# Performance work log

Hardware: AMD Instinct MI355X
Metric: run time of the kernel (lower is better)

Reference implementation:

```python
import jax, jax.numpy as jnp
import numpy as np

B, DIM = 16384, 1024
H1, H2, H3 = 500, 200, 200


def setup_inputs() -> dict:
    key = jax.random.key(0)
    ks = jax.random.split(key, 16)
    s = 0.01
    return {
        "x": jax.random.normal(ks[0], (B, DIM), dtype=jnp.float32),
        "show_index": jax.random.randint(ks[1], (B,), 0, 100),
        "st": jax.random.normal(ks[2], (1000, 16), dtype=jnp.float32),
        # deep MLP params (shared across the two task heads, as in the source)
        "W1": jax.random.normal(ks[3], (DIM, H1), dtype=jnp.float32) * s,
        "b1": jnp.zeros((H1,), dtype=jnp.float32),
        "W2": jax.random.normal(ks[4], (H1, H2), dtype=jnp.float32) * s,
        "b2": jnp.zeros((H2,), dtype=jnp.float32),
        "W3": jax.random.normal(ks[5], (H2, H3), dtype=jnp.float32) * s,
        "b3": jnp.zeros((H3,), dtype=jnp.float32),
        # final sigmoid head on concat([emb(DIM), d3(H3)])
        "Wl": jax.random.normal(ks[6], (DIM + H3, 1), dtype=jnp.float32) * s,
        "bl": jnp.zeros((1,), dtype=jnp.float32),
        # per-(task, cross-layer) cross weights/biases: tf.random_normal stddev=0.01
        "cw": jax.random.normal(ks[7], (2, 3, DIM), dtype=jnp.float32) * s,
        "cb": jax.random.normal(ks[8], (2, 3, DIM), dtype=jnp.float32) * s,
    }


def reference(x, show_index, st, W1, b1, W2, b2, W3, b3, Wl, bl, cw, cb):
    # Deep part (same shared Dense layers each task -> compute once).
    d = jax.nn.relu(x @ W1 + b1)
    d = jax.nn.relu(d @ W2 + b2)
    d3 = jax.nn.relu(d @ W3 + b3)  # (B, H3)

    # cross_net: sum_i w[j] * x[b,i] * emb[b,j]  ==  x.sum(1) * emb[b,j] * w[j]
    # (collapsed form of the (B,dim,dim) outer product + axis-1 reduction)
    xsum = jnp.sum(x, axis=1, keepdims=True)  # (B, 1)
    preds = []
    for i in range(2):
        emb = x
        for j in range(3):
            emb = xsum * emb * cw[i, j] + cb[i, j] + x
        mid = jnp.concatenate([emb, d3], axis=-1)  # (B, DIM+H3)
        preds.append(jax.nn.sigmoid(mid @ Wl + bl))  # (B, 1)
    return tuple(preds)
```

## Files before the change

kernel.cpp:

```cpp
#include <hip/hip_runtime.h>
#include <hip/hip_bf16.h>
#include <math.h>

#define B_ROWS 16384
#define DIM 1024

typedef __attribute__((ext_vector_type(8))) short s16x8;
typedef __attribute__((ext_vector_type(4))) float f32x4;

static __device__ __forceinline__ unsigned short f2bf(float f) {
    union { float f; unsigned u; } v; v.f = f;
    unsigned r = v.u + 0x7FFF + ((v.u >> 16) & 1);
    return (unsigned short)(r >> 16);
}

static __device__ __forceinline__ unsigned cvt_pk_bf16(float lo, float hi) {
    unsigned r;
    asm volatile("v_cvt_pk_bf16_f32 %0, %1, %2" : "=v"(r) : "v"(lo), "v"(hi));
    return r;
}

static __device__ __forceinline__ void gload16(const unsigned short* g, unsigned short* l) {
    __builtin_amdgcn_global_load_lds(
        (const __attribute__((address_space(1))) unsigned int*)g,
        (__attribute__((address_space(3))) unsigned int*)l, 16, 0, 0);
}

__global__ __launch_bounds__(256) void prep(
    const float* __restrict__ W1, const float* __restrict__ W2,
    const float* __restrict__ W3,
    const float* __restrict__ cw, const float* __restrict__ cb,
    const float* __restrict__ Wl,
    unsigned short* __restrict__ W1b, unsigned short* __restrict__ W2b,
    unsigned short* __restrict__ W3b,
    float* __restrict__ czz) {
    __shared__ unsigned short tile[64][72];
    __shared__ float red[4][6];
    const int tid = threadIdx.x;
    const int blk = blockIdx.x;

    if (blk < 176) {
        const int w = blk;
        const float* src; unsigned short* dst;
        int kt, nt, Ksrc, Nsrc, ldDst;
        bool skipHi = false;
        if (w < 128)      { kt = w & 15;         nt = w >> 4;         src = W1; dst = W1b; Ksrc = 1024; Nsrc = 500; ldDst = 1024; skipHi = true; }
        else if (w < 160) { kt = (w - 128) & 7;  nt = (w - 128) >> 3; src = W2; dst = W2b; Ksrc = 500;  Nsrc = 200; ldDst = 512;  }
        else              { kt = (w - 160) & 3;  nt = (w - 160) >> 2; src = W3; dst = W3b; Ksrc = 200;  Nsrc = 200; ldDst = 256;  }
        const int k0 = kt << 6, n0 = nt << 6;
        {
            const int r = tid >> 2, c0 = (tid & 3) << 4;
            const int kk = k0 + r;
#pragma unroll
            for (int i = 0; i < 16; ++i) {
                const int nn = n0 + c0 + i;
                const float v = (kk < Ksrc && nn < Nsrc) ? src[(size_t)kk * Nsrc + nn] : 0.f;
                tile[r][c0 + i] = f2bf(v);
            }
        }
        __syncthreads();
        {
            const int n = tid >> 2, kc = (tid & 3) << 4;
            if (!(skipHi && (n0 + n) >= 500)) {
                unsigned short* o = dst + (size_t)(n0 + n) * ldDst + k0 + kc;
#pragma unroll
                for (int i = 0; i < 16; ++i) o[i] = tile[kc + i][n];
            }
        }
    } else if (blk == 176) {
#pragma unroll
        for (int q = 0; q < 4; ++q) {
            const int k = tid * 4 + q;
            const float wl = Wl[k];
            const float a1 = cw[k],         a2 = cw[1024 + k],  a3 = cw[2048 + k];
            const float d1_ = cw[3072 + k], d2_ = cw[4096 + k], d3_ = cw[5120 + k];
            W1b[(size_t)500 * 1024 + k] = f2bf(a1 * a2 * a3 * wl);
            W1b[(size_t)501 * 1024 + k] = f2bf(a2 * a3 * wl);
            W1b[(size_t)502 * 1024 + k] = f2bf(a3 * wl);
            W1b[(size_t)503 * 1024 + k] = f2bf(d1_ * d2_ * d3_ * wl);
            W1b[(size_t)504 * 1024 + k] = f2bf(d2_ * d3_ * wl);
            W1b[(size_t)505 * 1024 + k] = f2bf(d3_ * wl);
            W1b[(size_t)506 * 1024 + k] = f2bf(wl);
            W1b[(size_t)507 * 1024 + k] = 0x3F80;
            W1b[(size_t)508 * 1024 + k] = 0;
            W1b[(size_t)509 * 1024 + k] = 0;
            W1b[(size_t)510 * 1024 + k] = 0;
            W1b[(size_t)511 * 1024 + k] = 0;
        }
    } else {
        float c[6] = {0.f, 0.f, 0.f, 0.f, 0.f, 0.f};
#pragma unroll
        for (int q = 0; q < 4; ++q) {
            const int k = tid * 4 + q;
            const float wl = Wl[k];
            {
                const float w2 = cw[1024 + k], w3 = cw[2048 + k];
                const float b1 = cb[k], b2 = cb[1024 + k], b3 = cb[2048 + k];
                c[0] += w2 * w3 * b1 * wl;
                c[1] += w3 * b2 * wl;
                c[2] += b3 * wl;
            }
            {
                const float w2 = cw[4096 + k], w3 = cw[5120 + k];
                const float b1 = cb[3072 + k], b2 = cb[4096 + k], b3 = cb[5120 + k];
                c[3] += w2 * w3 * b1 * wl;
                c[4] += w3 * b2 * wl;
                c[5] += b3 * wl;
            }
        }
        const int lane = tid & 63, wv = tid >> 6;
#pragma unroll
        for (int j = 0; j < 6; ++j)
#pragma unroll
            for (int m = 1; m < 64; m <<= 1) c[j] += __shfl_xor(c[j], m, 64);
        if (lane == 0)
#pragma unroll
            for (int j = 0; j < 6; ++j) red[wv][j] = c[j];
        __syncthreads();
        if (tid < 6) czz[tid] = red[0][tid] + red[1][tid] + red[2][tid] + red[3][tid];
    }
}

template <int ROWS>
static __device__ __forceinline__ void stage8(
    const unsigned short* __restrict__ src, int K, int rowBase, int kt,
    unsigned short* lds, int w, int lane) {
    const int r8   = lane >> 3;
    const int slot = lane & 7;
#pragma unroll
    for (int q = 0; q < ROWS / 64; ++q) {
        const int blk   = q * 8 + w;
        const int row   = blk * 8 + r8;
        const int chunk = slot ^ (row & 7);
        const unsigned short* g = src + (size_t)(rowBase + row) * K + kt * 64 + chunk * 8;
        gload16(g, lds + blk * 512);
    }
}

__global__ __launch_bounds__(512, 4) void gemm_xa(
    const float* __restrict__ X,
    const unsigned short* __restrict__ Bw,
    const float* __restrict__ bias,
    unsigned short* __restrict__ C,
    float* __restrict__ zparts) {
    constexpr int K = 1024, ldc = 512, nK = 16;
    __shared__ unsigned short As[2][128 * 64];
    __shared__ unsigned short Bs[3][128 * 64];

    const int tid  = threadIdx.x;
    const int lane = tid & 63;
    const int wid  = tid >> 6;
    const int wm   = wid >> 2;
    const int wn   = wid & 3;
    const int g    = lane >> 4;
    const int r16  = lane & 15;

    const int cpx = gridDim.x >> 3;
    const int swz = (blockIdx.x & 7) * cpx + (blockIdx.x >> 3);
    const int rowBase = (swz >> 2) << 7;
    const int colBase = (swz & 3) << 7;

    const int arow = tid >> 2;
    const float* aSrc = X + (size_t)(rowBase + arow) * K + ((tid & 3) << 4);

    float4 bank0[4], bank1[4];

    f32x4 acc[4][2];
#pragma unroll
    for (int m = 0; m < 4; ++m)
#pragma unroll
        for (int n = 0; n < 2; ++n)
            acc[m][n] = (f32x4){0.f, 0.f, 0.f, 0.f};

#define ISSUE_A(kt_, bank_)                                                   \
    {                                                                         \
        _Pragma("unroll")                                                     \
        for (int q = 0; q < 4; ++q)                                           \
            bank_[q] = *(const float4*)(aSrc + (kt_) * 64 + q * 4);           \
    }

#define CVT_WRITE_A(bank_, dst_)                                              \
    {                                                                         \
        const int cb_ = (tid & 3) << 1;                                       \
        uint4 v0_, v1_;                                                       \
        v0_.x = cvt_pk_bf16(bank_[0].x, bank_[0].y);                          \
        v0_.y = cvt_pk_bf16(bank_[0].z, bank_[0].w);                          \
        v0_.z = cvt_pk_bf16(bank_[1].x, bank_[1].y);                          \
        v0_.w = cvt_pk_bf16(bank_[1].z, bank_[1].w);                          \
        v1_.x = cvt_pk_bf16(bank_[2].x, bank_[2].y);                          \
        v1_.y = cvt_pk_bf16(bank_[2].z, bank_[2].w);                          \
        v1_.z = cvt_pk_bf16(bank_[3].x, bank_[3].y);                          \
        v1_.w = cvt_pk_bf16(bank_[3].z, bank_[3].w);                          \
        const int ch0_ = (cb_ + 0) ^ (arow & 7);                              \
        const int ch1_ = (cb_ + 1) ^ (arow & 7);                              \
        *(uint4*)((char*)(dst_) + arow * 128 + ch0_ * 16) = v0_;              \
        *(uint4*)((char*)(dst_) + arow * 128 + ch1_ * 16) = v1_;              \
    }

    ISSUE_A(0, bank0);
    asm volatile("" ::: "memory");
    ISSUE_A(1, bank1);
    asm volatile("" ::: "memory");
    stage8<128>(Bw, K, colBase, 0, Bs[0], wid, lane);
    stage8<128>(Bw, K, colBase, 1, Bs[1], wid, lane);
    asm volatile("" ::: "memory");
    CVT_WRITE_A(bank0, As[0]);
    asm volatile("s_waitcnt vmcnt(2)" ::: "memory");
    asm volatile("s_waitcnt lgkmcnt(0)" ::: "memory");
    __builtin_amdgcn_s_barrier();
    asm volatile("" ::: "memory");

    for (int kt = 0; kt < nK; ++kt) {
        const unsigned short* Ab = As[kt & 1];
        const unsigned short* Bb = Bs[kt % 3];

        if (kt + 2 < nK) {
            if ((kt & 1) == 0) { ISSUE_A(kt + 2, bank0); }
            else               { ISSUE_A(kt + 2, bank1); }
            asm volatile("" ::: "memory");
            stage8<128>(Bw, K, colBase, kt + 2, Bs[(kt + 2) % 3], wid, lane);
            asm volatile("" ::: "memory");
        }

#pragma unroll
        for (int ks = 0; ks < 2; ++ks) {
            s16x8 af[4], bfr[2];
#pragma unroll
            for (int m = 0; m < 4; ++m) {
                const int row = wm * 64 + m * 16 + r16;
                const int off = ((ks * 4 + g) * 16) ^ ((row & 7) << 4);
                af[m] = *(const s16x8*)((const char*)Ab + row * 128 + off);
            }
#pragma unroll
            for (int n = 0; n < 2; ++n) {
                const int row = wn * 32 + n * 16 + r16;
                const int off = ((ks * 4 + g) * 16) ^ ((row & 7) << 4);
                bfr[n] = *(const s16x8*)((const char*)Bb + row * 128 + off);
            }
#pragma unroll
            for (int m = 0; m < 4; ++m)
#pragma unroll
                for (int n = 0; n < 2; ++n)
                    acc[m][n] = __builtin_amdgcn_mfma_f32_16x16x32_bf16(af[m], bfr[n], acc[m][n], 0, 0, 0);
        }

        if (kt + 1 < nK) {
            if ((kt & 1) == 0) { CVT_WRITE_A(bank1, As[1]); }
            else               { CVT_WRITE_A(bank0, As[0]); }
        }

        if (kt + 2 < nK)
            asm volatile("s_waitcnt vmcnt(6)" ::: "memory");
        else
            asm volatile("s_waitcnt vmcnt(0)" ::: "memory");
        asm volatile("s_waitcnt lgkmcnt(0)" ::: "memory");
        __builtin_amdgcn_s_barrier();
        asm volatile("" ::: "memory");
    }
#undef ISSUE_A
#undef CVT_WRITE_A

    unsigned short* Cb = As[0];
#pragma unroll
    for (int n = 0; n < 2; ++n) {
        const int lcol = wn * 32 + n * 16 + r16;
        const int col = colBase + lcol;
        const float bv = (col < 500) ? bias[col] : 0.f;
        const unsigned pc = (unsigned)(col - 500);
#pragma unroll
        for (int m = 0; m < 4; ++m) {
            const int lrow = wm * 64 + m * 16 + g * 4;
#pragma unroll
            for (int r = 0; r < 4; ++r) {
                const float raw = acc[m][n][r];
                if (pc < 8u) zparts[(size_t)(rowBase + lrow + r) * 8 + pc] = raw;
                float v = raw + bv;
                v = v > 0.f ? v : 0.f;
                Cb[(lrow + r) * 128 + lcol] = f2bf(v);
            }
        }
    }
    __syncthreads();

    {
        const int row = tid >> 2;
        const int q   = tid & 3;
        const uint4* s = (const uint4*)(Cb + row * 128 + q * 32);
        uint4* d = (uint4*)(C + (size_t)(rowBase + row) * ldc + colBase + q * 32);
        d[0] = s[0];
        d[1] = s[1];
    }
}

__global__ __launch_bounds__(512) void tail_fused(
    const unsigned short* __restrict__ d1,
    const unsigned short* __restrict__ W2b,
    const float* __restrict__ b2,
    const unsigned short* __restrict__ W3b,
    const float* __restrict__ b3,
    const float* __restrict__ Wl,
    const float* __restrict__ bl,
    const float* __restrict__ zparts,
    const float* __restrict__ czz,
    float* __restrict__ out) {
    __shared__ unsigned short As[2][64 * 64];
    __shared__ unsigned short Bs[2][256 * 64];
    __shared__ unsigned short P[64 * 256];
    __shared__ float part[8][64];

    const int tid  = threadIdx.x;
    const int lane = tid & 63;
    const int wid  = tid >> 6;
    const int wm   = wid >> 2;
    const int wn   = wid & 3;
    const int g    = lane >> 4;
    const int r16  = lane & 15;
    const int rowBase = blockIdx.x << 6;

    f32x4 acc[2][4];
#pragma unroll
    for (int m = 0; m < 2; ++m)
#pragma unroll
        for (int n = 0; n < 4; ++n)
            acc[m][n] = (f32x4){0.f, 0.f, 0.f, 0.f};

    stage8<64>(d1, 512, rowBase, 0, As[0], wid, lane);
    stage8<256>(W2b, 512, 0, 0, Bs[0], wid, lane);

    for (int kt = 0; kt < 8; ++kt) {
        const int buf = kt & 1;
        if (kt + 1 < 8) {
            stage8<64>(d1, 512, rowBase, kt + 1, As[buf ^ 1], wid, lane);
            stage8<256>(W2b, 512, 0, kt + 1, Bs[buf ^ 1], wid, lane);
            asm volatile("s_waitcnt vmcnt(5)" ::: "memory");
        } else {
            asm volatile("s_waitcnt vmcnt(0)" ::: "memory");
        }
        __builtin_amdgcn_s_barrier();
        asm volatile("" ::: "memory");

        const unsigned short* Ab = As[buf];
        const unsigned short* Bb = Bs[buf];
#pragma unroll
        for (int ks = 0; ks < 2; ++ks) {
            s16x8 af[2], bfr[4];
#pragma unroll
            for (int m = 0; m < 2; ++m) {
                const int row = wm * 32 + m * 16 + r16;
                const int off = ((ks * 4 + g) * 16) ^ ((row & 7) << 4);
                af[m] = *(const s16x8*)((const char*)Ab + row * 128 + off);
            }
#pragma unroll
            for (int n = 0; n < 4; ++n) {
                const int row = wn * 64 + n * 16 + r16;
                const int off = ((ks * 4 + g) * 16) ^ ((row & 7) << 4);
                bfr[n] = *(const s16x8*)((const char*)Bb + row * 128 + off);
            }
#pragma unroll
            for (int m = 0; m < 2; ++m)
#pragma unroll
                for (int n = 0; n < 4; ++n)
                    acc[m][n] = __builtin_amdgcn_mfma_f32_16x16x32_bf16(af[m], bfr[n], acc[m][n], 0, 0, 0);
        }
        asm volatile("s_waitcnt lgkmcnt(0)" ::: "memory");
        __builtin_amdgcn_s_barrier();
        asm volatile("" ::: "memory");
    }

#pragma unroll
    for (int n = 0; n < 4; ++n) {
        const int col = wn * 64 + n * 16 + r16;
        const float bv = (col < 200) ? b2[col] : 0.f;
#pragma unroll
        for (int m = 0; m < 2; ++m) {
#pragma unroll
            for (int r = 0; r < 4; ++r) {
                const int row = wm * 32 + m * 16 + g * 4 + r;
                float v = acc[m][n][r] + bv;
                v = v > 0.f ? v : 0.f;
                const int byte = row * 512 + ((col * 2) ^ ((row & 7) << 4));
                *(unsigned short*)((char*)P + byte) = f2bf(v);
            }
        }
    }

    stage8<256>(W3b, 256, 0, 0, Bs[0], wid, lane);
    asm volatile("s_waitcnt lgkmcnt(0)" ::: "memory");
    __builtin_amdgcn_s_barrier();
    asm volatile("" ::: "memory");

    f32x4 acc2[2][4];
#pragma unroll
    for (int m = 0; m < 2; ++m)
#pragma unroll
        for (int n = 0; n < 4; ++n)
            acc2[m][n] = (f32x4){0.f, 0.f, 0.f, 0.f};

    for (int kt = 0; kt < 4; ++kt) {
        const int buf = kt & 1;
        if (kt + 1 < 4) {
            stage8<256>(W3b, 256, 0, kt + 1, Bs[buf ^ 1], wid, lane);
            asm volatile("s_waitcnt vmcnt(4)" ::: "memory");
        } else {
            asm volatile("s_waitcnt vmcnt(0)" ::: "memory");
        }
        __builtin_amdgcn_s_barrier();
        asm volatile("" ::: "memory");

        const unsigned short* Bb = Bs[buf];
#pragma unroll
        for (int ks = 0; ks < 2; ++ks) {
            s16x8 af[2], bfr[4];
#pragma unroll
            for (int m = 0; m < 2; ++m) {
                const int row = wm * 32 + m * 16 + r16;
                const int byte = row * 512 + ((kt * 128 + (ks * 4 + g) * 16) ^ ((row & 7) << 4));
                af[m] = *(const s16x8*)((const char*)P + byte);
            }
#pragma unroll
            for (int n = 0; n < 4; ++n) {
                const int row = wn * 64 + n * 16 + r16;
                const int off = ((ks * 4 + g) * 16) ^ ((row & 7) << 4);
                bfr[n] = *(const s16x8*)((const char*)Bb + row * 128 + off);
            }
#pragma unroll
            for (int m = 0; m < 2; ++m)
#pragma unroll
                for (int n = 0; n < 4; ++n)
                    acc2[m][n] = __builtin_amdgcn_mfma_f32_16x16x32_bf16(af[m], bfr[n], acc2[m][n], 0, 0, 0);
        }
        asm volatile("s_waitcnt lgkmcnt(0)" ::: "memory");
        __builtin_amdgcn_s_barrier();
        asm volatile("" ::: "memory");
    }

    float wlv[4], b3v[4];
#pragma unroll
    for (int n = 0; n < 4; ++n) {
        const int col = wn * 64 + n * 16 + r16;
        wlv[n] = (col < 200) ? Wl[1024 + col] : 0.f;
        b3v[n] = (col < 200) ? b3[col] : 0.f;
    }
#pragma unroll
    for (int m = 0; m < 2; ++m) {
#pragma unroll
        for (int r = 0; r < 4; ++r) {
            float s = 0.f;
#pragma unroll
            for (int n = 0; n < 4; ++n) {
                float v = acc2[m][n][r] + b3v[n];
                v = v > 0.f ? v : 0.f;
                s += v * wlv[n];
            }
            s += __shfl_xor(s, 1, 64);
            s += __shfl_xor(s, 2, 64);
            s += __shfl_xor(s, 4, 64);
            s += __shfl_xor(s, 8, 64);
            if (r16 == 0) part[wid][wm * 32 + m * 16 + g * 4 + r] = s;
        }
    }
    __syncthreads();

    if (tid < 64) {
        const int row = rowBase + tid;
        const int wmr = (tid >> 5) << 2;
        const float t = part[wmr][tid] + part[wmr + 1][tid] +
                        part[wmr + 2][tid] + part[wmr + 3][tid];
        const float blv = bl[0];
        const float* zp = zparts + (size_t)row * 8;
        float4 zpa = *(const float4*)(zp);
        float4 zpb = *(const float4*)(zp + 4);
        const float s = zpb.w;
        const float z0 = ((zpa.x * s + zpa.y + czz[0]) * s + zpa.z + czz[1]) * s
                         + zpb.z + czz[2] + t + blv;
        const float z1 = ((zpa.w * s + zpb.x + czz[3]) * s + zpb.y + czz[4]) * s
                         + zpb.z + czz[5] + t + blv;
        out[row]          = 1.f / (1.f + expf(-z0));
        out[B_ROWS + row] = 1.f / (1.f + expf(-z1));
    }
}

extern "C" void kernel_launch(void* const* d_in, const int* in_sizes, int n_in,
                              void* d_out, int out_size, void* d_ws, size_t ws_size,
                              hipStream_t stream) {
    const float* x  = (const float*)d_in[0];
    const float* W1 = (const float*)d_in[3];
    const float* b1 = (const float*)d_in[4];
    const float* W2 = (const float*)d_in[5];
    const float* b2 = (const float*)d_in[6];
    const float* W3 = (const float*)d_in[7];
    const float* b3 = (const float*)d_in[8];
    const float* Wl = (const float*)d_in[9];
    const float* bl = (const float*)d_in[10];
    const float* cw = (const float*)d_in[11];
    const float* cb = (const float*)d_in[12];
    float* out = (float*)d_out;

    unsigned short* d1  = (unsigned short*)d_ws;
    unsigned short* W1b = d1 + (size_t)16384 * 512;
    unsigned short* W2b = W1b + (size_t)512 * 1024;
    unsigned short* W3b = W2b + (size_t)256 * 512;
    float* zparts = (float*)(W3b + (size_t)256 * 256);
    float* czz = zparts + (size_t)16384 * 8;

    prep<<<178, 256, 0, stream>>>(W1, W2, W3, cw, cb, Wl, W1b, W2b, W3b, czz);

    gemm_xa<<<512, 512, 0, stream>>>(x, W1b, b1, d1, zparts);

    tail_fused<<<256, 512, 0, stream>>>(d1, W2b, b2, W3b, b3, Wl, bl,
                                        zparts, czz, out);
}
```

Before: 55.56 us.

## Retile first GEMM to 64x512 blocks so fp32 X is read once

```diff
diff --git a/kernel.cpp b/kernel.cpp
--- a/kernel.cpp
+++ b/kernel.cpp
@@ -137,72 +137,59 @@
     }
 }
 
-__global__ __launch_bounds__(512, 4) void gemm_xa(
+__global__ __launch_bounds__(512, 2) void gemm_xa(
     const float* __restrict__ X,
     const unsigned short* __restrict__ Bw,
     const float* __restrict__ bias,
     unsigned short* __restrict__ C,
     float* __restrict__ zparts) {
-    constexpr int K = 1024, ldc = 512, nK = 16;
-    __shared__ unsigned short As[2][128 * 64];
-    __shared__ unsigned short Bs[3][128 * 64];
+    constexpr int K = 1024, nK = 16;
+    __shared__ unsigned short As[2][64 * 64];
+    __shared__ unsigned short Bs[2][512 * 64];
 
     const int tid  = threadIdx.x;
     const int lane = tid & 63;
     const int wid  = tid >> 6;
-    const int wm   = wid >> 2;
-    const int wn   = wid & 3;
     const int g    = lane >> 4;
     const int r16  = lane & 15;
 
-    const int cpx = gridDim.x >> 3;
-    const int swz = (blockIdx.x & 7) * cpx + (blockIdx.x >> 3);
-    const int rowBase = (swz >> 2) << 7;
-    const int colBase = (swz & 3) << 7;
-
-    const int arow = tid >> 2;
-    const float* aSrc = X + (size_t)(rowBase + arow) * K + ((tid & 3) << 4);
-
-    float4 bank0[4], bank1[4];
-
-    f32x4 acc[4][2];
+    const int rowBase = blockIdx.x << 6;
+
+    const int arow = tid >> 3;
+    const int ak8  = tid & 7;
+    const float* aSrc = X + (size_t)(rowBase + arow) * K + ak8 * 8;
+
+    float4 bank0[2], bank1[2];
+
+    f32x4 acc[4][4];
 #pragma unroll
     for (int m = 0; m < 4; ++m)
 #pragma unroll
-        for (int n = 0; n < 2; ++n)
+        for (int n = 0; n < 4; ++n)
             acc[m][n] = (f32x4){0.f, 0.f, 0.f, 0.f};
 
 #define ISSUE_A(kt_, bank_)                                                   \
     {                                                                         \
-        _Pragma("unroll")                                                     \
-        for (int q = 0; q < 4; ++q)                                           \
-            bank_[q] = *(const float4*)(aSrc + (kt_) * 64 + q * 4);           \
+        bank_[0] = *(const float4*)(aSrc + (kt_) * 64);                       \
+        bank_[1] = *(const float4*)(aSrc + (kt_) * 64 + 4);                   \
     }
 
 #define CVT_WRITE_A(bank_, dst_)                                              \
     {                                                                         \
-        const int cb_ = (tid & 3) << 1;                                       \
-        uint4 v0_, v1_;                                                       \
-        v0_.x = cvt_pk_bf16(bank_[0].x, bank_[0].y);                          \
-        v0_.y = cvt_pk_bf16(bank_[0].z, bank_[0].w);                          \
-        v0_.z = cvt_pk_bf16(bank_[1].x, bank_[1].y);                          \
-        v0_.w = cvt_pk_bf16(bank_[1].z, bank_[1].w);                          \
-        v1_.x = cvt_pk_bf16(bank_[2].x, bank_[2].y);                          \
-        v1_.y = cvt_pk_bf16(bank_[2].z, bank_[2].w);                          \
-        v1_.z = cvt_pk_bf16(bank_[3].x, bank_[3].y);                          \
-        v1_.w = cvt_pk_bf16(bank_[3].z, bank_[3].w);                          \
-        const int ch0_ = (cb_ + 0) ^ (arow & 7);                              \
-        const int ch1_ = (cb_ + 1) ^ (arow & 7);                              \
-        *(uint4*)((char*)(dst_) + arow * 128 + ch0_ * 16) = v0_;              \
-        *(uint4*)((char*)(dst_) + arow * 128 + ch1_ * 16) = v1_;              \
-    }
-
+        uint4 v_;                                                             \
+        v_.x = cvt_pk_bf16(bank_[0].x, bank_[0].y);                           \
+        v_.y = cvt_pk_bf16(bank_[0].z, bank_[0].w);                           \
+        v_.z = cvt_pk_bf16(bank_[1].x, bank_[1].y);                           \
+        v_.w = cvt_pk_bf16(bank_[1].z, bank_[1].w);                           \
+        const int ch_ = ak8 ^ (arow & 7);                                     \
+        *(uint4*)((char*)(dst_) + arow * 128 + ch_ * 16) = v_;                \
+    }
+
+    stage8<512>(Bw, K, 0, 0, Bs[0], wid, lane);
+    asm volatile("" ::: "memory");
     ISSUE_A(0, bank0);
     asm volatile("" ::: "memory");
     ISSUE_A(1, bank1);
-    asm volatile("" ::: "memory");
-    stage8<128>(Bw, K, colBase, 0, Bs[0], wid, lane);
-    stage8<128>(Bw, K, colBase, 1, Bs[1], wid, lane);
     asm volatile("" ::: "memory");
     CVT_WRITE_A(bank0, As[0]);
     asm volatile("s_waitcnt vmcnt(2)" ::: "memory");
@@ -212,35 +199,37 @@
 
     for (int kt = 0; kt < nK; ++kt) {
         const unsigned short* Ab = As[kt & 1];
-        const unsigned short* Bb = Bs[kt % 3];
-
+        const unsigned short* Bb = Bs[kt & 1];
+
+        if (kt + 1 < nK) {
+            stage8<512>(Bw, K, 0, kt + 1, Bs[(kt + 1) & 1], wid, lane);
+            asm volatile("" ::: "memory");
+        }
         if (kt + 2 < nK) {
             if ((kt & 1) == 0) { ISSUE_A(kt + 2, bank0); }
             else               { ISSUE_A(kt + 2, bank1); }
             asm volatile("" ::: "memory");
-            stage8<128>(Bw, K, colBase, kt + 2, Bs[(kt + 2) % 3], wid, lane);
-            asm volatile("" ::: "memory");
         }
 
 #pragma unroll
         for (int ks = 0; ks < 2; ++ks) {
-            s16x8 af[4], bfr[2];
+            s16x8 af[4], bfr[4];
 #pragma unroll
             for (int m = 0; m < 4; ++m) {
-                const int row = wm * 64 + m * 16 + r16;
+                const int row = m * 16 + r16;
                 const int off = ((ks * 4 + g) * 16) ^ ((row & 7) << 4);
                 af[m] = *(const s16x8*)((const char*)Ab + row * 128 + off);
             }
 #pragma unroll
-            for (int n = 0; n < 2; ++n) {
-                const int row = wn * 32 + n * 16 + r16;
+            for (int n = 0; n < 4; ++n) {
+                const int row = wid * 64 + n * 16 + r16;
                 const int off = ((ks * 4 + g) * 16) ^ ((row & 7) << 4);
                 bfr[n] = *(const s16x8*)((const char*)Bb + row * 128 + off);
             }
 #pragma unroll
             for (int m = 0; m < 4; ++m)
 #pragma unroll
-                for (int n = 0; n < 2; ++n)
+                for (int n = 0; n < 4; ++n)
                     acc[m][n] = __builtin_amdgcn_mfma_f32_16x16x32_bf16(af[m], bfr[n], acc[m][n], 0, 0, 0);
         }
 
@@ -250,7 +239,7 @@
         }
 
         if (kt + 2 < nK)
-            asm volatile("s_waitcnt vmcnt(6)" ::: "memory");
+            asm volatile("s_waitcnt vmcnt(2)" ::: "memory");
         else
             asm volatile("s_waitcnt vmcnt(0)" ::: "memory");
         asm volatile("s_waitcnt lgkmcnt(0)" ::: "memory");
@@ -260,35 +249,34 @@
 #undef ISSUE_A
 #undef CVT_WRITE_A
 
-    unsigned short* Cb = As[0];
-#pragma unroll
-    for (int n = 0; n < 2; ++n) {
-        const int lcol = wn * 32 + n * 16 + r16;
-        const int col = colBase + lcol;
+    unsigned short* Cb = Bs[0];
+#pragma unroll
+    for (int n = 0; n < 4; ++n) {
+        const int col = wid * 64 + n * 16 + r16;
         const float bv = (col < 500) ? bias[col] : 0.f;
         const unsigned pc = (unsigned)(col - 500);
 #pragma unroll
         for (int m = 0; m < 4; ++m) {
-            const int lrow = wm * 64 + m * 16 + g * 4;
+            const int lrow = m * 16 + g * 4;
 #pragma unroll
             for (int r = 0; r < 4; ++r) {
                 const float raw = acc[m][n][r];
                 if (pc < 8u) zparts[(size_t)(rowBase + lrow + r) * 8 + pc] = raw;
                 float v = raw + bv;
                 v = v > 0.f ? v : 0.f;
-                Cb[(lrow + r) * 128 + lcol] = f2bf(v);
+                Cb[(lrow + r) * 512 + col] = f2bf(v);
             }
         }
     }
     __syncthreads();
 
     {
-        const int row = tid >> 2;
-        const int q   = tid & 3;
-        const uint4* s = (const uint4*)(Cb + row * 128 + q * 32);
-        uint4* d = (uint4*)(C + (size_t)(rowBase + row) * ldc + colBase + q * 32);
-        d[0] = s[0];
-        d[1] = s[1];
+        const int row = tid >> 3;
+        const int seg = tid & 7;
+        const uint4* s = (const uint4*)(Cb + row * 512 + seg * 64);
+        uint4* d = (uint4*)(C + (size_t)(rowBase + row) * 512 + seg * 64);
+#pragma unroll
+        for (int i = 0; i < 8; ++i) d[i] = s[i];
     }
 }
 
@@ -505,7 +493,7 @@
 
     prep<<<178, 256, 0, stream>>>(W1, W2, W3, cw, cb, Wl, W1b, W2b, W3b, czz);
 
-    gemm_xa<<<512, 512, 0, stream>>>(x, W1b, b1, d1, zparts);
+    gemm_xa<<<256, 512, 0, stream>>>(x, W1b, b1, d1, zparts);
 
     tail_fused<<<256, 512, 0, stream>>>(d1, W2b, b2, W3b, b3, Wl, bl,
                                         zparts, czz, out);
```

New measurement: 60.85 us. 1.1x slower.
